# Kernel tuning notes

Hardware: AMD Instinct MI355X
Metric: run time of the kernel (lower is better)

## Reference

```python
import jax, jax.numpy as jnp
import numpy as np

IN_DIM = 32768
OUT_DIM = 32768
BATCH = 1024


def setup_inputs() -> dict:
    key = jax.random.key(0)
    k1, k2, k3, k4 = jax.random.split(key, 4)
    x = jax.random.uniform(k1, (BATCH, IN_DIM), dtype=jnp.float32)
    negation_logits = jax.random.normal(k2, (OUT_DIM, 2), dtype=jnp.float32)
    idx_a = jax.random.randint(k3, (OUT_DIM,), 0, IN_DIM, dtype=jnp.int64)
    idx_b = jax.random.randint(k4, (OUT_DIM,), 0, IN_DIM, dtype=jnp.int64)
    return {"x": x, "negation_logits": negation_logits, "idx_a": idx_a, "idx_b": idx_b}


def reference(x, negation_logits, idx_a, idx_b):
    # Gather the two fan-in wires of every AND gate: [B, out_dim]
    a = x[:, idx_a]
    b = x[:, idx_b]
    # Hard negation flags from learned logits (straight-through: forward value is hard).
    p = jax.nn.sigmoid(negation_logits)  # [out_dim, 2]
    flag = p > 0.5
    a_mod = jnp.where(flag[:, 0][None, :], 1.0 - a, a)
    b_mod = jnp.where(flag[:, 1][None, :], 1.0 - b, b)
    return a_mod * b_mod  # soft AND gate
```

## Files before the change

### kernel.cpp

```cpp
#include <hip/hip_runtime.h>
#include <stdint.h>

#define IN_DIM  32768
#define OUT_DIM 32768
#define BATCH   1024
#define NT      1024
#define ITER    (OUT_DIM / 4 / NT)

typedef float fvec4 __attribute__((ext_vector_type(4)));

__device__ __forceinline__ uint32_t f32_to_bf16_bits(float f) {
    uint32_t u = __builtin_bit_cast(uint32_t, f);
    return (u + 0x7FFFu + ((u >> 16) & 1u)) >> 16;
}

__global__ void pack_meta(const int* __restrict__ idx_a,
                          const int* __restrict__ idx_b,
                          const float* __restrict__ logits,
                          uint32_t* __restrict__ packed) {
    int j = blockIdx.x * blockDim.x + threadIdx.x;
    if (j >= OUT_DIM) return;
    uint32_t ia = (((uint32_t)idx_a[j]) << 1) & 0xFFFFu;
    uint32_t ib = (((uint32_t)idx_b[j]) << 1) & 0xFFFFu;
    if (logits[2 * j + 0] > 0.0f) ia |= 1u;
    if (logits[2 * j + 1] > 0.0f) ib |= 1u;
    packed[j] = ia | (ib << 16);
}

__device__ __forceinline__ float ldrow(const uint16_t* row, uint32_t byteoff) {
    uint16_t h = *(const uint16_t*)((const char*)row + byteoff);
    return __builtin_bit_cast(float, ((uint32_t)h) << 16);
}
__device__ __forceinline__ float sel(uint32_t flag, float v) {
    return flag ? 1.0f - v : v;
}

__global__ __launch_bounds__(NT, 8) void logic_gather(
        const float* __restrict__ x,
        const uint32_t* __restrict__ packed,
        float* __restrict__ out) {
    __shared__ __align__(16) uint16_t row[IN_DIM];
    const int r = blockIdx.x;
    const int t = threadIdx.x;

    const float4* __restrict__ xrow = (const float4*)(x + (size_t)r * IN_DIM);
    uint2* __restrict__ row64 = (uint2*)row;
#pragma unroll
    for (int i = 0; i < IN_DIM / 4 / NT; ++i) {
        int e4 = i * NT + t;
        float4 v = xrow[e4];
        uint2 h;
        h.x = f32_to_bf16_bits(v.x) | (f32_to_bf16_bits(v.y) << 16);
        h.y = f32_to_bf16_bits(v.z) | (f32_to_bf16_bits(v.w) << 16);
        row64[e4] = h;
    }

    const uint4* __restrict__ pk = (const uint4*)packed;
    uint4 p[ITER];
#pragma unroll
    for (int i = 0; i < ITER; ++i) p[i] = pk[i * NT + t];

    __syncthreads();

    fvec4* __restrict__ orow = (fvec4*)(out + (size_t)r * OUT_DIM);
#pragma unroll
    for (int i = 0; i < ITER; ++i) {
        const uint32_t w0 = p[i].x, w1 = p[i].y, w2 = p[i].z, w3 = p[i].w;
        float a0 = ldrow(row, w0 & 0xFFFEu), b0 = ldrow(row, (w0 >> 16) & 0xFFFEu);
        float a1 = ldrow(row, w1 & 0xFFFEu), b1 = ldrow(row, (w1 >> 16) & 0xFFFEu);
        float a2 = ldrow(row, w2 & 0xFFFEu), b2 = ldrow(row, (w2 >> 16) & 0xFFFEu);
        float a3 = ldrow(row, w3 & 0xFFFEu), b3 = ldrow(row, (w3 >> 16) & 0xFFFEu);
        fvec4 res;
        res.x = sel(w0 & 1u, a0) * sel(w0 & 0x10000u, b0);
        res.y = sel(w1 & 1u, a1) * sel(w1 & 0x10000u, b1);
        res.z = sel(w2 & 1u, a2) * sel(w2 & 0x10000u, b2);
        res.w = sel(w3 & 1u, a3) * sel(w3 & 0x10000u, b3);
        __builtin_nontemporal_store(res, &orow[i * NT + t]);
    }
}

extern "C" void kernel_launch(void* const* d_in, const int* in_sizes, int n_in,
                              void* d_out, int out_size, void* d_ws, size_t ws_size,
                              hipStream_t stream) {
    const float* x      = (const float*)d_in[0];
    const float* logits = (const float*)d_in[1];
    const int*   idx_a  = (const int*)d_in[2];
    const int*   idx_b  = (const int*)d_in[3];
    uint32_t*    packed = (uint32_t*)d_ws;
    float*       out    = (float*)d_out;

    hipLaunchKernelGGL(pack_meta, dim3(OUT_DIM / 256), dim3(256), 0, stream,
                       idx_a, idx_b, logits, packed);
    hipLaunchKernelGGL(logic_gather, dim3(BATCH), dim3(NT), 0, stream,
                       x, packed, out);
}
```

Baseline: 242.7 us.

## Make gather kernel persistent with double-buffered row prefetch

Launches 256 blocks, each handling 4 batch rows, instead of one block per row. The next row of x is prefetched into registers while the current row is gathered, then converted to bf16 into a second LDS buffer. The packed metadata is loaded once per block rather than once per row. This hides the global load latency behind the gather work, at the cost of twice the LDS per block, more registers, lower occupancy and fewer blocks than CUs. It also replaces nontemporal output stores with normal stores.

```diff
diff --git a/kernel.cpp b/kernel.cpp
--- a/kernel.cpp
+++ b/kernel.cpp
@@ -6,8 +6,8 @@
 #define BATCH   1024
 #define NT      1024
 #define ITER    (OUT_DIM / 4 / NT)
-
-typedef float fvec4 __attribute__((ext_vector_type(4)));
+#define NBLK    256
+#define ROWS_PER_BLK (BATCH / NBLK)
 
 __device__ __forceinline__ uint32_t f32_to_bf16_bits(float f) {
     uint32_t u = __builtin_bit_cast(uint32_t, f);
@@ -35,47 +35,78 @@
     return flag ? 1.0f - v : v;
 }
 
-__global__ __launch_bounds__(NT, 8) void logic_gather(
+__global__ __launch_bounds__(NT, 4) void logic_gather(
         const float* __restrict__ x,
         const uint32_t* __restrict__ packed,
         float* __restrict__ out) {
-    __shared__ __align__(16) uint16_t row[IN_DIM];
-    const int r = blockIdx.x;
+    __shared__ __align__(16) uint16_t rows[2][IN_DIM];
     const int t = threadIdx.x;
-
-    const float4* __restrict__ xrow = (const float4*)(x + (size_t)r * IN_DIM);
-    uint2* __restrict__ row64 = (uint2*)row;
-#pragma unroll
-    for (int i = 0; i < IN_DIM / 4 / NT; ++i) {
-        int e4 = i * NT + t;
-        float4 v = xrow[e4];
-        uint2 h;
-        h.x = f32_to_bf16_bits(v.x) | (f32_to_bf16_bits(v.y) << 16);
-        h.y = f32_to_bf16_bits(v.z) | (f32_to_bf16_bits(v.w) << 16);
-        row64[e4] = h;
-    }
 
     const uint4* __restrict__ pk = (const uint4*)packed;
     uint4 p[ITER];
 #pragma unroll
     for (int i = 0; i < ITER; ++i) p[i] = pk[i * NT + t];
 
+    int r = blockIdx.x;
+    {
+        const float4* __restrict__ xr = (const float4*)(x + (size_t)r * IN_DIM);
+        uint2* __restrict__ dst = (uint2*)rows[0];
+#pragma unroll
+        for (int i = 0; i < 8; ++i) {
+            int e4 = i * NT + t;
+            float4 v = xr[e4];
+            uint2 h;
+            h.x = f32_to_bf16_bits(v.x) | (f32_to_bf16_bits(v.y) << 16);
+            h.y = f32_to_bf16_bits(v.z) | (f32_to_bf16_bits(v.w) << 16);
+            dst[e4] = h;
+        }
+    }
     __syncthreads();
 
-    fvec4* __restrict__ orow = (fvec4*)(out + (size_t)r * OUT_DIM);
 #pragma unroll
-    for (int i = 0; i < ITER; ++i) {
-        const uint32_t w0 = p[i].x, w1 = p[i].y, w2 = p[i].z, w3 = p[i].w;
-        float a0 = ldrow(row, w0 & 0xFFFEu), b0 = ldrow(row, (w0 >> 16) & 0xFFFEu);
-        float a1 = ldrow(row, w1 & 0xFFFEu), b1 = ldrow(row, (w1 >> 16) & 0xFFFEu);
-        float a2 = ldrow(row, w2 & 0xFFFEu), b2 = ldrow(row, (w2 >> 16) & 0xFFFEu);
-        float a3 = ldrow(row, w3 & 0xFFFEu), b3 = ldrow(row, (w3 >> 16) & 0xFFFEu);
-        fvec4 res;
-        res.x = sel(w0 & 1u, a0) * sel(w0 & 0x10000u, b0);
-        res.y = sel(w1 & 1u, a1) * sel(w1 & 0x10000u, b1);
-        res.z = sel(w2 & 1u, a2) * sel(w2 & 0x10000u, b2);
-        res.w = sel(w3 & 1u, a3) * sel(w3 & 0x10000u, b3);
-        __builtin_nontemporal_store(res, &orow[i * NT + t]);
+    for (int k = 0; k < ROWS_PER_BLK; ++k) {
+        const int cur = k & 1;
+        const int rnext = r + NBLK;
+        const bool have_next = (k + 1 < ROWS_PER_BLK);
+
+        float4 nv[8];
+        if (have_next) {
+            const float4* __restrict__ xn = (const float4*)(x + (size_t)rnext * IN_DIM);
+#pragma unroll
+            for (int i = 0; i < 8; ++i) nv[i] = xn[i * NT + t];
+        }
+
+        const uint16_t* __restrict__ rowbuf = rows[cur];
+        float4* __restrict__ orow = (float4*)(out + (size_t)r * OUT_DIM);
+#pragma unroll
+        for (int i = 0; i < ITER; ++i) {
+            const uint32_t w0 = p[i].x, w1 = p[i].y, w2 = p[i].z, w3 = p[i].w;
+            float a0 = ldrow(rowbuf, w0 & 0xFFFEu), b0 = ldrow(rowbuf, (w0 >> 16) & 0xFFFEu);
+            float a1 = ldrow(rowbuf, w1 & 0xFFFEu), b1 = ldrow(rowbuf, (w1 >> 16) & 0xFFFEu);
+            float a2 = ldrow(rowbuf, w2 & 0xFFFEu), b2 = ldrow(rowbuf, (w2 >> 16) & 0xFFFEu);
+            float a3 = ldrow(rowbuf, w3 & 0xFFFEu), b3 = ldrow(rowbuf, (w3 >> 16) & 0xFFFEu);
+            float4 res;
+            res.x = sel(w0 & 1u, a0) * sel(w0 & 0x10000u, b0);
+            res.y = sel(w1 & 1u, a1) * sel(w1 & 0x10000u, b1);
+            res.z = sel(w2 & 1u, a2) * sel(w2 & 0x10000u, b2);
+            res.w = sel(w3 & 1u, a3) * sel(w3 & 0x10000u, b3);
+            orow[i * NT + t] = res;
+        }
+
+        if (have_next) {
+            uint2* __restrict__ dst = (uint2*)rows[cur ^ 1];
+#pragma unroll
+            for (int i = 0; i < 8; ++i) {
+                int e4 = i * NT + t;
+                uint2 h;
+                h.x = f32_to_bf16_bits(nv[i].x) | (f32_to_bf16_bits(nv[i].y) << 16);
+                h.y = f32_to_bf16_bits(nv[i].z) | (f32_to_bf16_bits(nv[i].w) << 16);
+                dst[e4] = h;
+            }
+        }
+
+        __syncthreads();
+        r = rnext;
     }
 }
 
@@ -91,6 +122,6 @@
 
     hipLaunchKernelGGL(pack_meta, dim3(OUT_DIM / 256), dim3(256), 0, stream,
                        idx_a, idx_b, logits, packed);
-    hipLaunchKernelGGL(logic_gather, dim3(BATCH), dim3(NT), 0, stream,
+    hipLaunchKernelGGL(logic_gather, dim3(NBLK), dim3(NT), 0, stream,
                        x, packed, out);
 }
```

After: 257.7 us. +6.1%, slower.
